# Kernel tuning notes

Hardware: AMD Instinct MI355X
Metric: run time of the kernel (lower is better)

The kernel has to match this reference:

```python
import jax, jax.numpy as jnp
import numpy as np

N = 8192        # total mesh nodes
M1 = 6000       # nodes set from x (full 3D coords)
M2 = 2000       # nodes set from y (coords 0 and 2 only)
B = 4           # batch
K = 4           # smoothing steps


def setup_inputs() -> dict:
    key = jax.random.key(0)
    k1, k2, k3, k4 = jax.random.split(key, 4)
    # Sparse-ish random symmetric-flavored adjacency, stored dense (as the module does).
    A = (jax.random.uniform(k1, (N, N)) < 0.002).astype(jnp.float32)
    idx = jnp.arange(N)
    # Ring edges guarantee every row has degree >= 1 (avoid divide-by-zero).
    A = A.at[idx, (idx + 1) % N].set(1.0)
    A = A.at[(idx + 1) % N, idx].set(1.0)
    # Diagonal: 1 for first half, 0 for second half -> output mask selects N//2 nodes.
    A = A.at[idx, idx].set((idx < N // 2).astype(jnp.float32))
    # Disjoint index sets for the scatter writes.
    perm = jax.random.permutation(k2, N)
    li1 = perm[:M1].astype(jnp.int64)
    li2 = perm[M1:M1 + M2].astype(jnp.int64)
    x = jax.random.normal(k3, (B, M1 * 3), dtype=jnp.float32)
    y = jax.random.normal(k4, (B, M2 * 2), dtype=jnp.float32)
    temp_zero = jnp.zeros((N, 3), dtype=jnp.float32)
    return {"x": x, "y": y, "edge_matrix": A, "temp_zero": temp_zero,
            "local_indices_1": li1, "local_indices_2": li2, "k": K}


def reference(x, y, edge_matrix, temp_zero, local_indices_1, local_indices_2, k):
    b = x.shape[0]
    # Scatter-build the graph state [B, N, 3].
    temp = jnp.broadcast_to(temp_zero[None], (b,) + temp_zero.shape)
    temp = temp.at[:, local_indices_1, :].set(x.reshape(b, -1, 3))
    y2 = y.reshape(b, -1, 2)
    temp = temp.at[:, local_indices_2, 0].set(y2[:, :, 0])
    temp = temp.at[:, local_indices_2, 2].set(y2[:, :, 1])
    # Degree normalization vector (row sums), computed once.
    deg = jnp.sum(edge_matrix, axis=1)  # [N]
    mesh = temp
    for _ in range(k):
        # smoother: (mesh^T @ A^T)^T == A @ mesh over the node dim, then /degree.
        mesh = jnp.einsum('ij,bjc->bic', edge_matrix, mesh) / deg[None, :, None]
    # Gather rows whose diagonal adjacency entry is zero.
    mask = jnp.diag(edge_matrix) == 0
    return mesh[:, mask, :]
```

## Files before the change

kernel.cpp:

```cpp
#include <hip/hip_runtime.h>

#define NN   8192
#define NNP  (NN + 4)
#define NN3  (NN * 3)
#define NNP3 (NNP * 3)
#define CAP  64
#define M1   6000
#define M2   2000
#define SENT NN
#define CT   256
#define SB   64
#define NPS  (NN / SB)

typedef unsigned short u16;
typedef float f4v __attribute__((ext_vector_type(4)));

__global__ __launch_bounds__(256) void build_ell(const float* __restrict__ A,
                                                 u16* __restrict__ cols,
                                                 int* __restrict__ nch,
                                                 float* __restrict__ rdeg,
                                                 const int* __restrict__ li1,
                                                 const int* __restrict__ li2,
                                                 const float* __restrict__ x,
                                                 const float* __restrict__ y,
                                                 float* __restrict__ mesh_a,
                                                 float* __restrict__ mesh_b,
                                                 int B) {
    const int tid = threadIdx.x;
    __shared__ u16 enc16[NN];
    __shared__ int cnt;

    if (blockIdx.x >= NN) {
        const int sid = blockIdx.x - NN;
        for (int i = tid; i < NN; i += 256) enc16[i] = 0;
        __syncthreads();
        for (int j = tid; j < M1; j += 256) enc16[li1[j]] = (u16)(1 + j);
        for (int j = tid; j < M2; j += 256) enc16[li2[j]] = (u16)(M1 + 1 + j);
        __syncthreads();
        if (sid == 0 && tid < B * 12) {
            const int b = tid / 12, r = tid - b * 12;
            mesh_a[b * NNP3 + NN * 3 + r] = 0.f;
            mesh_b[b * NNP3 + NN * 3 + r] = 0.f;
        }
        const int lo = sid * NPS;
        for (int t = tid; t < B * NPS * 3; t += 256) {
            const int b  = t / (NPS * 3);
            const int rc = t - b * (NPS * 3);
            const int i  = lo + rc / 3, c = rc % 3;
            const u16 e  = enc16[i];
            float v = 0.f;
            if (e) {
                if (e <= M1)      v = x[(b * M1 + (e - 1)) * 3 + c];
                else if (c != 1)  v = y[(b * M2 + (e - (M1 + 1))) * 2 + (c >> 1)];
            }
            mesh_a[b * NNP3 + lo * 3 + rc] = v;
        }
        return;
    }

    const int row = blockIdx.x;
    if (tid == 0) cnt = 0;
    __syncthreads();
    const f4v* __restrict__ Arow = (const f4v*)(A + (size_t)row * NN);
    f4v v[8];
    #pragma unroll
    for (int k = 0; k < 8; ++k)
        v[k] = __builtin_nontemporal_load(&Arow[k * 256 + tid]);
    u16* __restrict__ crow = cols + row * CAP;
    #pragma unroll
    for (int k = 0; k < 8; ++k) {
        const int base = (k * 256 + tid) * 4;
        if (v[k].x != 0.f) { int p = atomicAdd(&cnt, 1); if (p < CAP) crow[p] = (u16)(base);     }
        if (v[k].y != 0.f) { int p = atomicAdd(&cnt, 1); if (p < CAP) crow[p] = (u16)(base + 1); }
        if (v[k].z != 0.f) { int p = atomicAdd(&cnt, 1); if (p < CAP) crow[p] = (u16)(base + 2); }
        if (v[k].w != 0.f) { int p = atomicAdd(&cnt, 1); if (p < CAP) crow[p] = (u16)(base + 3); }
    }
    __syncthreads();
    int c = cnt;
    if (c > CAP) c = CAP;
    const int padded = (c + 7) & ~7;
    if (tid < padded - c && c + tid < CAP) crow[c + tid] = (u16)SENT;
    if (tid == 0) {
        nch[row]  = padded >> 3;
        rdeg[row] = 1.0f / (float)cnt;
    }
}

#define GATHER8(mb)                                                             \
    { const uint4 q = cr[ch];                                                   \
      acc += mb[(q.x & 0xFFFF) * 3 + c] + mb[(q.x >> 16) * 3 + c]               \
           + mb[(q.y & 0xFFFF) * 3 + c] + mb[(q.y >> 16) * 3 + c]               \
           + mb[(q.z & 0xFFFF) * 3 + c] + mb[(q.z >> 16) * 3 + c]               \
           + mb[(q.w & 0xFFFF) * 3 + c] + mb[(q.w >> 16) * 3 + c]; }

__global__ __launch_bounds__(CT) void spmv_full(const u16* __restrict__ cols,
                                                const int* __restrict__ nch,
                                                const float* __restrict__ rdeg,
                                                const float* __restrict__ src,
                                                float* __restrict__ dst, int B) {
    const int g = blockIdx.x * CT + threadIdx.x;
    if (g >= B * NN3) return;
    const int b = g / NN3;
    const int r = g - b * NN3;
    const int i = r / 3, c = r - i * 3;
    const float* __restrict__ mb = src + b * NNP3;
    const uint4* __restrict__ cr = (const uint4*)(cols + i * CAP);
    const int n = nch[i];
    float acc = 0.f;
    for (int ch = 0; ch < n; ++ch) GATHER8(mb);
    dst[b * NNP3 + i * 3 + c] = acc * rdeg[i];
}

__global__ __launch_bounds__(CT) void spmv_last(const u16* __restrict__ cols,
                                                const int* __restrict__ nch,
                                                const float* __restrict__ rdeg,
                                                const float* __restrict__ src,
                                                float* __restrict__ out, int B) {
    const int H3 = (NN / 2) * 3;
    const int g = blockIdx.x * CT + threadIdx.x;
    if (g >= B * H3) return;
    const int b = g / H3;
    const int r = g - b * H3;
    const int i2 = r / 3, c = r - i2 * 3;
    const int i = NN / 2 + i2;
    const float* __restrict__ mb = src + b * NNP3;
    const uint4* __restrict__ cr = (const uint4*)(cols + i * CAP);
    const int n = nch[i];
    float acc = 0.f;
    for (int ch = 0; ch < n; ++ch) GATHER8(mb);
    out[g] = acc * rdeg[i];
}

extern "C" void kernel_launch(void* const* d_in, const int* in_sizes, int n_in,
                              void* d_out, int out_size, void* d_ws, size_t ws_size,
                              hipStream_t stream) {
    const float* x   = (const float*)d_in[0];
    const float* y   = (const float*)d_in[1];
    const float* A   = (const float*)d_in[2];
    const int*   li1 = (const int*)d_in[4];
    const int*   li2 = (const int*)d_in[5];

    const int B = in_sizes[0] / (M1 * 3);

    char* ws = (char*)d_ws;
    u16*   cols   = (u16*)ws;    ws += (size_t)NN * CAP * 2;
    int*   nchv   = (int*)ws;    ws += (size_t)NN * 4;
    float* rdeg   = (float*)ws;  ws += (size_t)NN * 4;
    float* mesh_a = (float*)ws;  ws += (size_t)B * NNP3 * 4;
    float* mesh_b = (float*)ws;

    build_ell<<<NN + SB, 256, 0, stream>>>(A, cols, nchv, rdeg,
                                           li1, li2, x, y, mesh_a, mesh_b, B);

    const int full = B * NN3;
    const int nbf = (full + CT - 1) / CT;
    spmv_full<<<nbf, CT, 0, stream>>>(cols, nchv, rdeg, mesh_a, mesh_b, B);
    spmv_full<<<nbf, CT, 0, stream>>>(cols, nchv, rdeg, mesh_b, mesh_a, B);
    spmv_full<<<nbf, CT, 0, stream>>>(cols, nchv, rdeg, mesh_a, mesh_b, B);

    const int half = B * (NN / 2) * 3;
    spmv_last<<<(half + CT - 1) / CT, CT, 0, stream>>>(cols, nchv, rdeg, mesh_b,
                                                       (float*)d_out, B);
}
```

Measured before the change: 69.06 us.

## Interleave batch and channel into 16-float node rows for coalesced gathers

Changes the mesh buffers from per-batch [B][N][3] to a node-major layout with a 16-float stride holding all 4 batches × 3 channels. Twelve consecutive threads now share one row's column list and gather neighbouring floats from one 64-byte segment. The aim is fewer scattered cache lines per gather and fewer redundant column-index loads across batches. It hardcodes B=4, since the stride of 16 only fits 12 values and the grid sizes no longer depend on B. It also pads each row with 4 unused floats.

Result: faster. 63.55 us (-8.0%).

```diff
diff --git a/kernel.cpp b/kernel.cpp
--- a/kernel.cpp
+++ b/kernel.cpp
@@ -1,9 +1,8 @@
 #include <hip/hip_runtime.h>
 
 #define NN   8192
-#define NNP  (NN + 4)
 #define NN3  (NN * 3)
-#define NNP3 (NNP * 3)
+#define ST   16
 #define CAP  64
 #define M1   6000
 #define M2   2000
@@ -37,23 +36,24 @@
         for (int j = tid; j < M1; j += 256) enc16[li1[j]] = (u16)(1 + j);
         for (int j = tid; j < M2; j += 256) enc16[li2[j]] = (u16)(M1 + 1 + j);
         __syncthreads();
-        if (sid == 0 && tid < B * 12) {
-            const int b = tid / 12, r = tid - b * 12;
-            mesh_a[b * NNP3 + NN * 3 + r] = 0.f;
-            mesh_b[b * NNP3 + NN * 3 + r] = 0.f;
+        if (sid == 0 && tid < ST) {
+            mesh_a[NN * ST + tid] = 0.f;
+            mesh_b[NN * ST + tid] = 0.f;
         }
         const int lo = sid * NPS;
-        for (int t = tid; t < B * NPS * 3; t += 256) {
-            const int b  = t / (NPS * 3);
-            const int rc = t - b * (NPS * 3);
-            const int i  = lo + rc / 3, c = rc % 3;
-            const u16 e  = enc16[i];
+        for (int t = tid; t < NPS * ST; t += 256) {
+            const int il = t >> 4, q = t & 15;
+            const int i = lo + il;
             float v = 0.f;
-            if (e) {
-                if (e <= M1)      v = x[(b * M1 + (e - 1)) * 3 + c];
-                else if (c != 1)  v = y[(b * M2 + (e - (M1 + 1))) * 2 + (c >> 1)];
+            if (q < 12) {
+                const u16 e = enc16[i];
+                if (e) {
+                    const int b = q / 3, c = q - b * 3;
+                    if (e <= M1)      v = x[(b * M1 + (e - 1)) * 3 + c];
+                    else if (c != 1)  v = y[(b * M2 + (e - (M1 + 1))) * 2 + (c >> 1)];
+                }
             }
-            mesh_a[b * NNP3 + lo * 3 + rc] = v;
+            mesh_a[(size_t)i * ST + q] = v;
         }
         return;
     }
@@ -88,47 +88,43 @@
 
 #define GATHER8(mb)                                                             \
     { const uint4 q = cr[ch];                                                   \
-      acc += mb[(q.x & 0xFFFF) * 3 + c] + mb[(q.x >> 16) * 3 + c]               \
-           + mb[(q.y & 0xFFFF) * 3 + c] + mb[(q.y >> 16) * 3 + c]               \
-           + mb[(q.z & 0xFFFF) * 3 + c] + mb[(q.z >> 16) * 3 + c]               \
-           + mb[(q.w & 0xFFFF) * 3 + c] + mb[(q.w >> 16) * 3 + c]; }
+      acc += mb[(q.x & 0xFFFF) * ST + bc] + mb[(q.x >> 16) * ST + bc]           \
+           + mb[(q.y & 0xFFFF) * ST + bc] + mb[(q.y >> 16) * ST + bc]           \
+           + mb[(q.z & 0xFFFF) * ST + bc] + mb[(q.z >> 16) * ST + bc]           \
+           + mb[(q.w & 0xFFFF) * ST + bc] + mb[(q.w >> 16) * ST + bc]; }
 
 __global__ __launch_bounds__(CT) void spmv_full(const u16* __restrict__ cols,
                                                 const int* __restrict__ nch,
                                                 const float* __restrict__ rdeg,
                                                 const float* __restrict__ src,
-                                                float* __restrict__ dst, int B) {
+                                                float* __restrict__ dst) {
     const int g = blockIdx.x * CT + threadIdx.x;
-    if (g >= B * NN3) return;
-    const int b = g / NN3;
-    const int r = g - b * NN3;
-    const int i = r / 3, c = r - i * 3;
-    const float* __restrict__ mb = src + b * NNP3;
+    const int i = g / 12, bc = g - (g / 12) * 12;
+    const int n = nch[i];
+    const float rd = rdeg[i];
     const uint4* __restrict__ cr = (const uint4*)(cols + i * CAP);
-    const int n = nch[i];
+    const float* __restrict__ mb = src;
     float acc = 0.f;
     for (int ch = 0; ch < n; ++ch) GATHER8(mb);
-    dst[b * NNP3 + i * 3 + c] = acc * rdeg[i];
+    dst[(size_t)i * ST + bc] = acc * rd;
 }
 
 __global__ __launch_bounds__(CT) void spmv_last(const u16* __restrict__ cols,
                                                 const int* __restrict__ nch,
                                                 const float* __restrict__ rdeg,
                                                 const float* __restrict__ src,
-                                                float* __restrict__ out, int B) {
-    const int H3 = (NN / 2) * 3;
+                                                float* __restrict__ out) {
     const int g = blockIdx.x * CT + threadIdx.x;
-    if (g >= B * H3) return;
-    const int b = g / H3;
-    const int r = g - b * H3;
-    const int i2 = r / 3, c = r - i2 * 3;
+    const int i2 = g / 12, bc = g - (g / 12) * 12;
+    const int b = bc / 3, c = bc - b * 3;
     const int i = NN / 2 + i2;
-    const float* __restrict__ mb = src + b * NNP3;
+    const int n = nch[i];
+    const float rd = rdeg[i];
     const uint4* __restrict__ cr = (const uint4*)(cols + i * CAP);
-    const int n = nch[i];
+    const float* __restrict__ mb = src;
     float acc = 0.f;
     for (int ch = 0; ch < n; ++ch) GATHER8(mb);
-    out[g] = acc * rdeg[i];
+    out[((size_t)b * (NN / 2) + i2) * 3 + c] = acc * rd;
 }
 
 extern "C" void kernel_launch(void* const* d_in, const int* in_sizes, int n_in,
@@ -146,19 +142,17 @@
     u16*   cols   = (u16*)ws;    ws += (size_t)NN * CAP * 2;
     int*   nchv   = (int*)ws;    ws += (size_t)NN * 4;
     float* rdeg   = (float*)ws;  ws += (size_t)NN * 4;
-    float* mesh_a = (float*)ws;  ws += (size_t)B * NNP3 * 4;
+    float* mesh_a = (float*)ws;  ws += (size_t)(NN + 1) * ST * 4;
     float* mesh_b = (float*)ws;
 
     build_ell<<<NN + SB, 256, 0, stream>>>(A, cols, nchv, rdeg,
                                            li1, li2, x, y, mesh_a, mesh_b, B);
 
-    const int full = B * NN3;
-    const int nbf = (full + CT - 1) / CT;
-    spmv_full<<<nbf, CT, 0, stream>>>(cols, nchv, rdeg, mesh_a, mesh_b, B);
-    spmv_full<<<nbf, CT, 0, stream>>>(cols, nchv, rdeg, mesh_b, mesh_a, B);
-    spmv_full<<<nbf, CT, 0, stream>>>(cols, nchv, rdeg, mesh_a, mesh_b, B);
+    const int nbf = NN * 12 / CT;
+    spmv_full<<<nbf, CT, 0, stream>>>(cols, nchv, rdeg, mesh_a, mesh_b);
+    spmv_full<<<nbf, CT, 0, stream>>>(cols, nchv, rdeg, mesh_b, mesh_a);
+    spmv_full<<<nbf, CT, 0, stream>>>(cols, nchv, rdeg, mesh_a, mesh_b);
 
-    const int half = B * (NN / 2) * 3;
-    spmv_last<<<(half + CT - 1) / CT, CT, 0, stream>>>(cols, nchv, rdeg, mesh_b,
-                                                       (float*)d_out, B);
+    const int nbl = (NN / 2) * 12 / CT;
+    spmv_last<<<nbl, CT, 0, stream>>>(cols, nchv, rdeg, mesh_b, (float*)d_out);
 }
```
